# Optimization experiments

Hardware: AMD Instinct MI355X
Metric: run time of the kernel (lower is better)

The kernel has to match this reference:

```python
import jax, jax.numpy as jnp
import numpy as np

B, T, IN, H, HH, OUT = 512, 512, 6, 64, 128, 8


def setup_inputs() -> dict:
    key = jax.random.key(0)
    ks = jax.random.split(key, 14)
    def lin(k, fan_in, shape):
        s = 1.0 / np.sqrt(fan_in)
        return jax.random.uniform(k, shape, jnp.float32, -s, s)
    return {
        "x": jax.random.normal(ks[0], (B, T, IN), jnp.float32),
        # initial_linear: input_dim -> hidden
        "W_init": lin(ks[1], IN, (IN, H)), "b_init": lin(ks[2], IN, (H,)),
        # vector-field MLP: hidden -> hh -> hh -> hh -> hidden*input
        "W_in": lin(ks[3], H, (H, HH)),  "b_in": lin(ks[4], H, (HH,)),
        "W_h1": lin(ks[5], HH, (HH, HH)), "b_h1": lin(ks[6], HH, (HH,)),
        "W_h2": lin(ks[7], HH, (HH, HH)), "b_h2": lin(ks[8], HH, (HH,)),
        "W_out": lin(ks[9], HH, (HH, H * IN)), "b_out": lin(ks[10], HH, (H * IN,)),
        # final linear: hidden -> output
        "W_fin": lin(ks[11], H, (H, OUT)), "b_fin": lin(ks[12], H, (OUT,)),
    }


def reference(x, W_init, b_init, W_in, b_in, W_h1, b_h1, W_h2, b_h2,
              W_out, b_out, W_fin, b_fin):
    # vector field: f(h) -> (B, H, IN) matrix; dh/dt = f(h) @ dX/dt
    def vf(h, dX):
        z = jax.nn.relu(h @ W_in + b_in)
        z = jax.nn.relu(z @ W_h1 + b_h1)
        z = jax.nn.relu(z @ W_h2 + b_h2)
        A = jnp.tanh(z @ W_out + b_out).reshape(h.shape[0], H, IN)
        return jnp.einsum("bhi,bi->bh", A, dX)

    # h0 from initial value of the path (spline.evaluate(0) == x[:, 0])
    h0 = x[:, 0] @ W_init + b_init  # (B, H)

    # linear interpolation: dX/dt constant on each unit interval
    dX = jnp.swapaxes(x[:, 1:] - x[:, :-1], 0, 1)  # (T-1, B, IN)

    def rk4_step(h, d):
        k1 = vf(h, d)
        k2 = vf(h + 0.5 * k1, d)
        k3 = vf(h + 0.5 * k2, d)
        k4 = vf(h + k3, d)
        h_new = h + (k1 + 2.0 * k2 + 2.0 * k3 + k4) / 6.0
        return h_new, h_new

    _, hs = jax.lax.scan(rk4_step, h0, dX)  # (T-1, B, H)
    hidden = jnp.concatenate([h0[None], hs], axis=0)  # (T, B, H)
    hidden = jnp.swapaxes(hidden, 0, 1)  # (B, T, H)

    # return_sequences=True -> final linear on all steps
    return hidden @ W_fin + b_fin  # (B, T, OUT)
```

## Files before the change

### kernel.cpp

```cpp
#include <hip/hip_runtime.h>
#include <stdint.h>

namespace {

constexpr int B_   = 512;
constexpr int T_   = 512;
constexpr int IN_  = 6;
constexpr int H_   = 64;
constexpr int HH_  = 128;
constexpr int OUT_ = 8;

typedef _Float16 f16x2 __attribute__((ext_vector_type(2)));

__device__ __forceinline__ float dot2f(uint32_t w, uint32_t z, float acc) {
#if __has_builtin(__builtin_amdgcn_fdot2)
    return __builtin_amdgcn_fdot2(__builtin_bit_cast(f16x2, w),
                                  __builtin_bit_cast(f16x2, z), acc, false);
#else
    f16x2 a = __builtin_bit_cast(f16x2, w);
    f16x2 b = __builtin_bit_cast(f16x2, z);
    return acc + (float)a[0] * (float)b[0] + (float)a[1] * (float)b[1];
#endif
}

__device__ __forceinline__ uint32_t pack2f(float a, float b) {
    f16x2 p;
    p[0] = (_Float16)a;
    p[1] = (_Float16)b;
    return __builtin_bit_cast(uint32_t, p);
}

__device__ __forceinline__ float tanh_fast(float v) {
    float ax = fabsf(v);
    float e  = __expf(2.0f * ax);
    float r  = 1.0f - 2.0f / (e + 1.0f);
    return copysignf(r, v);
}

__global__ __launch_bounds__(256, 2) void cde_kernel(
    const float* __restrict__ x,
    const float* __restrict__ W_init, const float* __restrict__ b_init,
    const float* __restrict__ W_in,   const float* __restrict__ b_in,
    const float* __restrict__ W_h1,   const float* __restrict__ b_h1,
    const float* __restrict__ W_h2,   const float* __restrict__ b_h2,
    const float* __restrict__ W_out,  const float* __restrict__ b_out,
    const float* __restrict__ W_fin,  const float* __restrict__ b_fin,
    float* __restrict__ out)
{
    const int b  = blockIdx.x;
    const int t  = threadIdx.x;
    const int c  = t >> 1;
    const int kh = t & 1;

    __shared__ alignas(16) uint32_t hin[H_ / 2];
    __shared__ alignas(16) uint32_t zA[HH_ / 2];
    __shared__ alignas(16) uint32_t zB[HH_ / 2];
    __shared__ alignas(16) float    pp[H_ * IN_];
    __shared__ float dxs[IN_];
    __shared__ float hbuf[H_];

    uint32_t w1[16], w2[32], w3[32], w4[96];
    #pragma unroll
    for (int i = 0; i < 16; ++i) {
        int k0 = kh * 32 + 2 * i;
        w1[i] = pack2f(W_in[k0 * HH_ + c], W_in[(k0 + 1) * HH_ + c]);
    }
    #pragma unroll
    for (int i = 0; i < 32; ++i) {
        int k0 = kh * 64 + 2 * i;
        w2[i] = pack2f(W_h1[k0 * HH_ + c], W_h1[(k0 + 1) * HH_ + c]);
        w3[i] = pack2f(W_h2[k0 * HH_ + c], W_h2[(k0 + 1) * HH_ + c]);
    }
    #pragma unroll
    for (int j = 0; j < 3; ++j) {
        const int cc = c + 128 * j;
        #pragma unroll
        for (int i = 0; i < 32; ++i) {
            int k0 = kh * 64 + 2 * i;
            w4[j * 32 + i] = pack2f(W_out[k0 * (H_ * IN_) + cc],
                                    W_out[(k0 + 1) * (H_ * IN_) + cc]);
        }
    }
    const float bin_r = b_in[c];
    const float bh1_r = b_h1[c];
    const float bh2_r = b_h2[c];
    const float bo0 = b_out[c], bo1 = b_out[c + 128], bo2 = b_out[c + 256];
    const int   m0 = c % 6, m1 = (c + 128) % 6, m2 = (c + 256) % 6;
    const float bfin_r = (t < OUT_) ? b_fin[t] : 0.0f;

    float wfr[8];
    #pragma unroll
    for (int j = 0; j < 8; ++j)
        wfr[j] = (t < 64) ? W_fin[((t >> 3) * 8 + j) * OUT_ + (t & 7)] : 0.0f;

    const size_t xbase = (size_t)b * T_ * IN_;
    const size_t obase = (size_t)b * T_ * OUT_;

    float xa = 0.f, xb = 0.f;
    if (t < IN_) {
        xa = x[xbase + t];
        xb = x[xbase + IN_ + t];
    }

    float h_reg = 0.f, hacc = 0.f;
    if (t < H_) {
        float s = b_init[t];
        #pragma unroll
        for (int i = 0; i < IN_; ++i) s += x[xbase + i] * W_init[i * H_ + t];
        h_reg = s;
        hbuf[t] = s;
        float o1 = __shfl_xor(s, 1);
        if ((t & 1) == 0) hin[t >> 1] = pack2f(s, o1);
    }
    __syncthreads();

    if (t < 64) {
        int o = t & 7, part = t >> 3;
        float s = 0.f;
        #pragma unroll
        for (int j = 0; j < 8; ++j) s += hbuf[part * 8 + j] * wfr[j];
        s += __shfl_xor(s, 8);
        s += __shfl_xor(s, 16);
        s += __shfl_xor(s, 32);
        if (part == 0) out[obase + o] = s + bfin_r;
    }

    for (int step = 0; step < T_ - 1; ++step) {
        if (t < IN_) {
            dxs[t] = xb - xa;
            xa = xb;
            if (step + 2 < T_) xb = x[xbase + (size_t)(step + 2) * IN_ + t];
        }

        #pragma unroll
        for (int s4 = 0; s4 < 4; ++s4) {
            float acc = 0.f;
            #pragma unroll
            for (int i = 0; i < 4; ++i) {
                uint4 zz = *reinterpret_cast<const uint4*>(&hin[kh * 16 + 4 * i]);
                acc = dot2f(w1[4 * i + 0], zz.x, acc);
                acc = dot2f(w1[4 * i + 1], zz.y, acc);
                acc = dot2f(w1[4 * i + 2], zz.z, acc);
                acc = dot2f(w1[4 * i + 3], zz.w, acc);
            }
            acc += __shfl_xor(acc, 1);
            float z  = fmaxf(bin_r + acc, 0.f);
            float zo = __shfl_xor(z, 2);
            if ((t & 3) == 0) zA[t >> 2] = pack2f(z, zo);
            __syncthreads();

            acc = 0.f;
            #pragma unroll
            for (int i = 0; i < 8; ++i) {
                uint4 zz = *reinterpret_cast<const uint4*>(&zA[kh * 32 + 4 * i]);
                acc = dot2f(w2[4 * i + 0], zz.x, acc);
                acc = dot2f(w2[4 * i + 1], zz.y, acc);
                acc = dot2f(w2[4 * i + 2], zz.z, acc);
                acc = dot2f(w2[4 * i + 3], zz.w, acc);
            }
            acc += __shfl_xor(acc, 1);
            z  = fmaxf(bh1_r + acc, 0.f);
            zo = __shfl_xor(z, 2);
            if ((t & 3) == 0) zB[t >> 2] = pack2f(z, zo);
            __syncthreads();

            acc = 0.f;
            #pragma unroll
            for (int i = 0; i < 8; ++i) {
                uint4 zz = *reinterpret_cast<const uint4*>(&zB[kh * 32 + 4 * i]);
                acc = dot2f(w3[4 * i + 0], zz.x, acc);
                acc = dot2f(w3[4 * i + 1], zz.y, acc);
                acc = dot2f(w3[4 * i + 2], zz.z, acc);
                acc = dot2f(w3[4 * i + 3], zz.w, acc);
            }
            acc += __shfl_xor(acc, 1);
            z  = fmaxf(bh2_r + acc, 0.f);
            zo = __shfl_xor(z, 2);
            if ((t & 3) == 0) zA[t >> 2] = pack2f(z, zo);
            __syncthreads();

            float a0 = 0.f, a1 = 0.f, a2 = 0.f;
            #pragma unroll
            for (int i = 0; i < 8; ++i) {
                uint4 zz = *reinterpret_cast<const uint4*>(&zA[kh * 32 + 4 * i]);
                a0 = dot2f(w4[4 * i + 0], zz.x, a0);
                a0 = dot2f(w4[4 * i + 1], zz.y, a0);
                a0 = dot2f(w4[4 * i + 2], zz.z, a0);
                a0 = dot2f(w4[4 * i + 3], zz.w, a0);
                a1 = dot2f(w4[32 + 4 * i + 0], zz.x, a1);
                a1 = dot2f(w4[32 + 4 * i + 1], zz.y, a1);
                a1 = dot2f(w4[32 + 4 * i + 2], zz.z, a1);
                a1 = dot2f(w4[32 + 4 * i + 3], zz.w, a1);
                a2 = dot2f(w4[64 + 4 * i + 0], zz.x, a2);
                a2 = dot2f(w4[64 + 4 * i + 1], zz.y, a2);
                a2 = dot2f(w4[64 + 4 * i + 2], zz.z, a2);
                a2 = dot2f(w4[64 + 4 * i + 3], zz.w, a2);
            }
            a0 += __shfl_xor(a0, 1);
            a1 += __shfl_xor(a1, 1);
            a2 += __shfl_xor(a2, 1);
            if ((t & 1) == 0) {
                pp[c]       = tanh_fast(bo0 + a0) * dxs[m0];
                pp[c + 128] = tanh_fast(bo1 + a1) * dxs[m1];
                pp[c + 256] = tanh_fast(bo2 + a2) * dxs[m2];
            }
            __syncthreads();

            if (t < H_) {
                const float* pr = &pp[t * 6];
                float kv = pr[0] + pr[1] + pr[2] + pr[3] + pr[4] + pr[5];
                hacc += ((s4 == 1 || s4 == 2) ? 2.0f : 1.0f) * kv;
                float hs;
                if (s4 < 3) {
                    hs = h_reg + ((s4 == 2) ? 1.0f : 0.5f) * kv;
                } else {
                    h_reg += hacc * (1.0f / 6.0f);
                    hacc = 0.f;
                    hbuf[t] = h_reg;
                    hs = h_reg;
                }
                float o1 = __shfl_xor(hs, 1);
                if ((t & 1) == 0) hin[t >> 1] = pack2f(hs, o1);
            }
            __syncthreads();
        }

        if (t < 64) {
            int o = t & 7, part = t >> 3;
            float s = 0.f;
            #pragma unroll
            for (int j = 0; j < 8; ++j) s += hbuf[part * 8 + j] * wfr[j];
            s += __shfl_xor(s, 8);
            s += __shfl_xor(s, 16);
            s += __shfl_xor(s, 32);
            if (part == 0) out[obase + (size_t)(step + 1) * OUT_ + o] = s + bfin_r;
        }
    }
}

}

extern "C" void kernel_launch(void* const* d_in, const int* in_sizes, int n_in,
                              void* d_out, int out_size, void* d_ws, size_t ws_size,
                              hipStream_t stream) {
    const float* x      = (const float*)d_in[0];
    const float* W_init = (const float*)d_in[1];
    const float* b_init = (const float*)d_in[2];
    const float* W_in   = (const float*)d_in[3];
    const float* b_in   = (const float*)d_in[4];
    const float* W_h1   = (const float*)d_in[5];
    const float* b_h1   = (const float*)d_in[6];
    const float* W_h2   = (const float*)d_in[7];
    const float* b_h2   = (const float*)d_in[8];
    const float* W_out  = (const float*)d_in[9];
    const float* b_out  = (const float*)d_in[10];
    const float* W_fin  = (const float*)d_in[11];
    const float* b_fin  = (const float*)d_in[12];
    float* out = (float*)d_out;

    cde_kernel<<<dim3(B_), dim3(256), 0, stream>>>(
        x, W_init, b_init, W_in, b_in, W_h1, b_h1, W_h2, b_h2,
        W_out, b_out, W_fin, b_fin, out);
}
```

Before: 3.605 ms.

## Split each MLP dot product across four lanes with 512-thread blocks

Doubles the block to 512 threads so each output column's reduction is split across four lanes instead of two. This halves per-thread weight registers and the serial dot-product chain, and uses DPP quad reductions in place of shuffles. Activations are now written as single fp16 values instead of packed pairs, and W_fin and b_out are moved into shared memory. The shorter per-step critical path should lower latency, at the cost of more waves per block and the same number of barriers per stage.

```diff
diff --git a/kernel.cpp b/kernel.cpp
--- a/kernel.cpp
+++ b/kernel.cpp
@@ -13,14 +13,8 @@
 typedef _Float16 f16x2 __attribute__((ext_vector_type(2)));
 
 __device__ __forceinline__ float dot2f(uint32_t w, uint32_t z, float acc) {
-#if __has_builtin(__builtin_amdgcn_fdot2)
     return __builtin_amdgcn_fdot2(__builtin_bit_cast(f16x2, w),
                                   __builtin_bit_cast(f16x2, z), acc, false);
-#else
-    f16x2 a = __builtin_bit_cast(f16x2, w);
-    f16x2 b = __builtin_bit_cast(f16x2, z);
-    return acc + (float)a[0] * (float)b[0] + (float)a[1] * (float)b[1];
-#endif
 }
 
 __device__ __forceinline__ uint32_t pack2f(float a, float b) {
@@ -30,6 +24,13 @@
     return __builtin_bit_cast(uint32_t, p);
 }
 
+__device__ __forceinline__ float qsum4(float v) {
+    int y = __builtin_amdgcn_mov_dpp(__builtin_bit_cast(int, v), 0xB1, 0xF, 0xF, true);
+    v += __builtin_bit_cast(float, y);
+    y = __builtin_amdgcn_mov_dpp(__builtin_bit_cast(int, v), 0x4E, 0xF, 0xF, true);
+    return v + __builtin_bit_cast(float, y);
+}
+
 __device__ __forceinline__ float tanh_fast(float v) {
     float ax = fabsf(v);
     float e  = __expf(2.0f * ax);
@@ -37,7 +38,7 @@
     return copysignf(r, v);
 }
 
-__global__ __launch_bounds__(256, 2) void cde_kernel(
+__global__ __launch_bounds__(512, 4) void cde_kernel(
     const float* __restrict__ x,
     const float* __restrict__ W_init, const float* __restrict__ b_init,
     const float* __restrict__ W_in,   const float* __restrict__ b_in,
@@ -49,49 +50,49 @@
 {
     const int b  = blockIdx.x;
     const int t  = threadIdx.x;
-    const int c  = t >> 1;
-    const int kh = t & 1;
-
-    __shared__ alignas(16) uint32_t hin[H_ / 2];
-    __shared__ alignas(16) uint32_t zA[HH_ / 2];
-    __shared__ alignas(16) uint32_t zB[HH_ / 2];
-    __shared__ alignas(16) float    pp[H_ * IN_];
+    const int c  = t >> 2;
+    const int kq = t & 3;
+
+    __shared__ alignas(16) uint32_t hinu[H_ / 2];
+    __shared__ alignas(16) uint32_t zAu[HH_ / 2];
+    __shared__ alignas(16) uint32_t zBu[HH_ / 2];
+    __shared__ alignas(16) float    pp[H_][8];
     __shared__ float dxs[IN_];
     __shared__ float hbuf[H_];
-
-    uint32_t w1[16], w2[32], w3[32], w4[96];
+    __shared__ float wfin_s[H_ * OUT_];
+    __shared__ float bfin_s[OUT_];
+    __shared__ float bo_s[3 * HH_];
+
+    uint32_t w1[8], w2[16], w3[16], w4[48];
+    #pragma unroll
+    for (int i = 0; i < 8; ++i) {
+        int k = kq * 16 + 2 * i;
+        w1[i] = pack2f(W_in[k * HH_ + c], W_in[(k + 1) * HH_ + c]);
+    }
     #pragma unroll
     for (int i = 0; i < 16; ++i) {
-        int k0 = kh * 32 + 2 * i;
-        w1[i] = pack2f(W_in[k0 * HH_ + c], W_in[(k0 + 1) * HH_ + c]);
-    }
-    #pragma unroll
-    for (int i = 0; i < 32; ++i) {
-        int k0 = kh * 64 + 2 * i;
-        w2[i] = pack2f(W_h1[k0 * HH_ + c], W_h1[(k0 + 1) * HH_ + c]);
-        w3[i] = pack2f(W_h2[k0 * HH_ + c], W_h2[(k0 + 1) * HH_ + c]);
+        int k = kq * 32 + 2 * i;
+        w2[i] = pack2f(W_h1[k * HH_ + c], W_h1[(k + 1) * HH_ + c]);
+        w3[i] = pack2f(W_h2[k * HH_ + c], W_h2[(k + 1) * HH_ + c]);
     }
     #pragma unroll
     for (int j = 0; j < 3; ++j) {
         const int cc = c + 128 * j;
         #pragma unroll
-        for (int i = 0; i < 32; ++i) {
-            int k0 = kh * 64 + 2 * i;
-            w4[j * 32 + i] = pack2f(W_out[k0 * (H_ * IN_) + cc],
-                                    W_out[(k0 + 1) * (H_ * IN_) + cc]);
+        for (int i = 0; i < 16; ++i) {
+            int k = kq * 32 + 2 * i;
+            w4[j * 16 + i] = pack2f(W_out[k * 384 + cc], W_out[(k + 1) * 384 + cc]);
         }
     }
     const float bin_r = b_in[c];
     const float bh1_r = b_h1[c];
     const float bh2_r = b_h2[c];
-    const float bo0 = b_out[c], bo1 = b_out[c + 128], bo2 = b_out[c + 256];
-    const int   m0 = c % 6, m1 = (c + 128) % 6, m2 = (c + 256) % 6;
-    const float bfin_r = (t < OUT_) ? b_fin[t] : 0.0f;
-
-    float wfr[8];
-    #pragma unroll
-    for (int j = 0; j < 8; ++j)
-        wfr[j] = (t < 64) ? W_fin[((t >> 3) * 8 + j) * OUT_ + (t & 7)] : 0.0f;
+    const int m0 = c % 6,          m1 = (c + 128) % 6,          m2 = (c + 256) % 6;
+    const int o0 = (c / 6) * 8 + m0, o1 = ((c + 128) / 6) * 8 + m1, o2 = ((c + 256) / 6) * 8 + m2;
+
+    wfin_s[t < H_ * OUT_ ? t : 0] = W_fin[t < H_ * OUT_ ? t : 0];
+    if (t < OUT_)     bfin_s[t] = b_fin[t];
+    if (t < 3 * HH_)  bo_s[t]   = b_out[t];
 
     const size_t xbase = (size_t)b * T_ * IN_;
     const size_t obase = (size_t)b * T_ * OUT_;
@@ -109,8 +110,7 @@
         for (int i = 0; i < IN_; ++i) s += x[xbase + i] * W_init[i * H_ + t];
         h_reg = s;
         hbuf[t] = s;
-        float o1 = __shfl_xor(s, 1);
-        if ((t & 1) == 0) hin[t >> 1] = pack2f(s, o1);
+        ((_Float16*)hinu)[t] = (_Float16)s;
     }
     __syncthreads();
 
@@ -118,11 +118,11 @@
         int o = t & 7, part = t >> 3;
         float s = 0.f;
         #pragma unroll
-        for (int j = 0; j < 8; ++j) s += hbuf[part * 8 + j] * wfr[j];
+        for (int j = 0; j < 8; ++j) s += hbuf[part * 8 + j] * wfin_s[(part * 8 + j) * OUT_ + o];
         s += __shfl_xor(s, 8);
         s += __shfl_xor(s, 16);
         s += __shfl_xor(s, 32);
-        if (part == 0) out[obase + o] = s + bfin_r;
+        if (part == 0) out[obase + o] = s + bfin_s[o];
     }
 
     for (int step = 0; step < T_ - 1; ++step) {
@@ -134,81 +134,111 @@
 
         #pragma unroll
         for (int s4 = 0; s4 < 4; ++s4) {
-            float acc = 0.f;
-            #pragma unroll
-            for (int i = 0; i < 4; ++i) {
-                uint4 zz = *reinterpret_cast<const uint4*>(&hin[kh * 16 + 4 * i]);
-                acc = dot2f(w1[4 * i + 0], zz.x, acc);
-                acc = dot2f(w1[4 * i + 1], zz.y, acc);
-                acc = dot2f(w1[4 * i + 2], zz.z, acc);
-                acc = dot2f(w1[4 * i + 3], zz.w, acc);
-            }
-            acc += __shfl_xor(acc, 1);
-            float z  = fmaxf(bin_r + acc, 0.f);
-            float zo = __shfl_xor(z, 2);
-            if ((t & 3) == 0) zA[t >> 2] = pack2f(z, zo);
-            __syncthreads();
-
-            acc = 0.f;
-            #pragma unroll
-            for (int i = 0; i < 8; ++i) {
-                uint4 zz = *reinterpret_cast<const uint4*>(&zA[kh * 32 + 4 * i]);
-                acc = dot2f(w2[4 * i + 0], zz.x, acc);
-                acc = dot2f(w2[4 * i + 1], zz.y, acc);
-                acc = dot2f(w2[4 * i + 2], zz.z, acc);
-                acc = dot2f(w2[4 * i + 3], zz.w, acc);
-            }
-            acc += __shfl_xor(acc, 1);
-            z  = fmaxf(bh1_r + acc, 0.f);
-            zo = __shfl_xor(z, 2);
-            if ((t & 3) == 0) zB[t >> 2] = pack2f(z, zo);
-            __syncthreads();
-
-            acc = 0.f;
-            #pragma unroll
-            for (int i = 0; i < 8; ++i) {
-                uint4 zz = *reinterpret_cast<const uint4*>(&zB[kh * 32 + 4 * i]);
-                acc = dot2f(w3[4 * i + 0], zz.x, acc);
-                acc = dot2f(w3[4 * i + 1], zz.y, acc);
-                acc = dot2f(w3[4 * i + 2], zz.z, acc);
-                acc = dot2f(w3[4 * i + 3], zz.w, acc);
-            }
-            acc += __shfl_xor(acc, 1);
-            z  = fmaxf(bh2_r + acc, 0.f);
-            zo = __shfl_xor(z, 2);
-            if ((t & 3) == 0) zA[t >> 2] = pack2f(z, zo);
-            __syncthreads();
-
-            float a0 = 0.f, a1 = 0.f, a2 = 0.f;
-            #pragma unroll
-            for (int i = 0; i < 8; ++i) {
-                uint4 zz = *reinterpret_cast<const uint4*>(&zA[kh * 32 + 4 * i]);
-                a0 = dot2f(w4[4 * i + 0], zz.x, a0);
-                a0 = dot2f(w4[4 * i + 1], zz.y, a0);
-                a0 = dot2f(w4[4 * i + 2], zz.z, a0);
-                a0 = dot2f(w4[4 * i + 3], zz.w, a0);
-                a1 = dot2f(w4[32 + 4 * i + 0], zz.x, a1);
-                a1 = dot2f(w4[32 + 4 * i + 1], zz.y, a1);
-                a1 = dot2f(w4[32 + 4 * i + 2], zz.z, a1);
-                a1 = dot2f(w4[32 + 4 * i + 3], zz.w, a1);
-                a2 = dot2f(w4[64 + 4 * i + 0], zz.x, a2);
-                a2 = dot2f(w4[64 + 4 * i + 1], zz.y, a2);
-                a2 = dot2f(w4[64 + 4 * i + 2], zz.z, a2);
-                a2 = dot2f(w4[64 + 4 * i + 3], zz.w, a2);
-            }
-            a0 += __shfl_xor(a0, 1);
-            a1 += __shfl_xor(a1, 1);
-            a2 += __shfl_xor(a2, 1);
-            if ((t & 1) == 0) {
-                pp[c]       = tanh_fast(bo0 + a0) * dxs[m0];
-                pp[c + 128] = tanh_fast(bo1 + a1) * dxs[m1];
-                pp[c + 256] = tanh_fast(bo2 + a2) * dxs[m2];
+            {
+                const uint32_t* hp = hinu + kq * 8;
+                uint4 q0 = *reinterpret_cast<const uint4*>(hp);
+                uint4 q1 = *reinterpret_cast<const uint4*>(hp + 4);
+                float a = 0.f, bq = 0.f;
+                a = dot2f(w1[0], q0.x, a); bq = dot2f(w1[1], q0.y, bq);
+                a = dot2f(w1[2], q0.z, a); bq = dot2f(w1[3], q0.w, bq);
+                a = dot2f(w1[4], q1.x, a); bq = dot2f(w1[5], q1.y, bq);
+                a = dot2f(w1[6], q1.z, a); bq = dot2f(w1[7], q1.w, bq);
+                float z = fmaxf(bin_r + qsum4(a + bq), 0.f);
+                if (kq == 0) ((_Float16*)zAu)[c] = (_Float16)z;
+            }
+            __syncthreads();
+
+            {
+                const uint32_t* zp = zAu + kq * 16;
+                uint4 q0 = *reinterpret_cast<const uint4*>(zp);
+                uint4 q1 = *reinterpret_cast<const uint4*>(zp + 4);
+                float a = 0.f, bq = 0.f;
+                a = dot2f(w2[0], q0.x, a); bq = dot2f(w2[1], q0.y, bq);
+                a = dot2f(w2[2], q0.z, a); bq = dot2f(w2[3], q0.w, bq);
+                a = dot2f(w2[4], q1.x, a); bq = dot2f(w2[5], q1.y, bq);
+                a = dot2f(w2[6], q1.z, a); bq = dot2f(w2[7], q1.w, bq);
+                uint4 q2 = *reinterpret_cast<const uint4*>(zp + 8);
+                uint4 q3 = *reinterpret_cast<const uint4*>(zp + 12);
+                a = dot2f(w2[8],  q2.x, a); bq = dot2f(w2[9],  q2.y, bq);
+                a = dot2f(w2[10], q2.z, a); bq = dot2f(w2[11], q2.w, bq);
+                a = dot2f(w2[12], q3.x, a); bq = dot2f(w2[13], q3.y, bq);
+                a = dot2f(w2[14], q3.z, a); bq = dot2f(w2[15], q3.w, bq);
+                float z = fmaxf(bh1_r + qsum4(a + bq), 0.f);
+                if (kq == 0) ((_Float16*)zBu)[c] = (_Float16)z;
+            }
+            __syncthreads();
+
+            {
+                const uint32_t* zp = zBu + kq * 16;
+                uint4 q0 = *reinterpret_cast<const uint4*>(zp);
+                uint4 q1 = *reinterpret_cast<const uint4*>(zp + 4);
+                float a = 0.f, bq = 0.f;
+                a = dot2f(w3[0], q0.x, a); bq = dot2f(w3[1], q0.y, bq);
+                a = dot2f(w3[2], q0.z, a); bq = dot2f(w3[3], q0.w, bq);
+                a = dot2f(w3[4], q1.x, a); bq = dot2f(w3[5], q1.y, bq);
+                a = dot2f(w3[6], q1.z, a); bq = dot2f(w3[7], q1.w, bq);
+                uint4 q2 = *reinterpret_cast<const uint4*>(zp + 8);
+                uint4 q3 = *reinterpret_cast<const uint4*>(zp + 12);
+                a = dot2f(w3[8],  q2.x, a); bq = dot2f(w3[9],  q2.y, bq);
+                a = dot2f(w3[10], q2.z, a); bq = dot2f(w3[11], q2.w, bq);
+                a = dot2f(w3[12], q3.x, a); bq = dot2f(w3[13], q3.y, bq);
+                a = dot2f(w3[14], q3.z, a); bq = dot2f(w3[15], q3.w, bq);
+                float z = fmaxf(bh2_r + qsum4(a + bq), 0.f);
+                if (kq == 0) ((_Float16*)zAu)[c] = (_Float16)z;
+            }
+            __syncthreads();
+
+            {
+                const uint32_t* zp = zAu + kq * 16;
+                uint4 q0 = *reinterpret_cast<const uint4*>(zp);
+                uint4 q1 = *reinterpret_cast<const uint4*>(zp + 4);
+                float a0 = 0.f, a1 = 0.f, a2 = 0.f;
+                #pragma unroll
+                for (int i = 0; i < 4; ++i) {
+                    uint32_t zi = (&q0.x)[i];
+                    a0 = dot2f(w4[i],      zi, a0);
+                    a1 = dot2f(w4[16 + i], zi, a1);
+                    a2 = dot2f(w4[32 + i], zi, a2);
+                }
+                #pragma unroll
+                for (int i = 0; i < 4; ++i) {
+                    uint32_t zi = (&q1.x)[i];
+                    a0 = dot2f(w4[4 + i],      zi, a0);
+                    a1 = dot2f(w4[20 + i], zi, a1);
+                    a2 = dot2f(w4[36 + i], zi, a2);
+                }
+                uint4 q2 = *reinterpret_cast<const uint4*>(zp + 8);
+                uint4 q3 = *reinterpret_cast<const uint4*>(zp + 12);
+                #pragma unroll
+                for (int i = 0; i < 4; ++i) {
+                    uint32_t zi = (&q2.x)[i];
+                    a0 = dot2f(w4[8 + i],      zi, a0);
+                    a1 = dot2f(w4[24 + i], zi, a1);
+                    a2 = dot2f(w4[40 + i], zi, a2);
+                }
+                #pragma unroll
+                for (int i = 0; i < 4; ++i) {
+                    uint32_t zi = (&q3.x)[i];
+                    a0 = dot2f(w4[12 + i],     zi, a0);
+                    a1 = dot2f(w4[28 + i], zi, a1);
+                    a2 = dot2f(w4[44 + i], zi, a2);
+                }
+                a0 = qsum4(a0);
+                a1 = qsum4(a1);
+                a2 = qsum4(a2);
+                if (kq == 0) {
+                    float* ppf = &pp[0][0];
+                    ppf[o0] = tanh_fast(bo_s[c]       + a0) * dxs[m0];
+                    ppf[o1] = tanh_fast(bo_s[c + 128] + a1) * dxs[m1];
+                    ppf[o2] = tanh_fast(bo_s[c + 256] + a2) * dxs[m2];
+                }
             }
             __syncthreads();
 
             if (t < H_) {
-                const float* pr = &pp[t * 6];
-                float kv = pr[0] + pr[1] + pr[2] + pr[3] + pr[4] + pr[5];
+                float4 p0 = *reinterpret_cast<const float4*>(&pp[t][0]);
+                float4 p1 = *reinterpret_cast<const float4*>(&pp[t][4]);
+                float kv = p0.x + p0.y + p0.z + p0.w + p1.x + p1.y;
                 hacc += ((s4 == 1 || s4 == 2) ? 2.0f : 1.0f) * kv;
                 float hs;
                 if (s4 < 3) {
@@ -219,8 +249,7 @@
                     hbuf[t] = h_reg;
                     hs = h_reg;
                 }
-                float o1 = __shfl_xor(hs, 1);
-                if ((t & 1) == 0) hin[t >> 1] = pack2f(hs, o1);
+                ((_Float16*)hinu)[t] = (_Float16)hs;
             }
             __syncthreads();
         }
@@ -229,11 +258,11 @@
             int o = t & 7, part = t >> 3;
             float s = 0.f;
             #pragma unroll
-            for (int j = 0; j < 8; ++j) s += hbuf[part * 8 + j] * wfr[j];
+            for (int j = 0; j < 8; ++j) s += hbuf[part * 8 + j] * wfin_s[(part * 8 + j) * OUT_ + o];
             s += __shfl_xor(s, 8);
             s += __shfl_xor(s, 16);
             s += __shfl_xor(s, 32);
-            if (part == 0) out[obase + (size_t)(step + 1) * OUT_ + o] = s + bfin_r;
+            if (part == 0) out[obase + (size_t)(step + 1) * OUT_ + o] = s + bfin_s[o];
         }
     }
 }
@@ -258,7 +287,7 @@
     const float* b_fin  = (const float*)d_in[12];
     float* out = (float*)d_out;
 
-    cde_kernel<<<dim3(B_), dim3(256), 0, stream>>>(
+    cde_kernel<<<dim3(B_), dim3(512), 0, stream>>>(
         x, W_init, b_init, W_in, b_in, W_h1, b_h1, W_h2, b_h2,
         W_out, b_out, W_fin, b_fin, out);
 }
```

Result: slower. 4.500 ms (+24.8%).
